# Performance work log

Measured on AMD Instinct MI355X. Metric: run time of the kernel, lower is better.

The kernel has to match this reference:

```python
import jax, jax.numpy as jnp
from jax import lax
import numpy as np

NUM_HEADS = 8
EPS = 1e-5


def _ln_c(x, g, b):
    # channel-first layernorm: x (B,C,S), normalize over C
    m = jnp.mean(x, axis=1, keepdims=True)
    v = jnp.var(x, axis=1, keepdims=True)
    return (x - m) / jnp.sqrt(v + EPS) * g[None, :, None] + b[None, :, None]


def _ln(x, g, b):
    m = jnp.mean(x, axis=-1, keepdims=True)
    v = jnp.var(x, axis=-1, keepdims=True)
    return (x - m) / jnp.sqrt(v + EPS) * g + b


def _sepconv(x, dw_w, dw_b, bn_s, bn_b, pw_w, pw_b, stride, pad):
    # depthwise conv -> eval BatchNorm (affine) -> ReLU -> pointwise conv
    C = x.shape[1]
    y = lax.conv_general_dilated(x, dw_w[:, None, :], (stride,), [(pad, pad)],
                                 dimension_numbers=('NCH', 'OIH', 'NCH'),
                                 feature_group_count=C)
    y = y + dw_b[None, :, None]
    y = jax.nn.relu(y * bn_s[None, :, None] + bn_b[None, :, None])
    return jnp.einsum('oc,bcs->bos', pw_w, y) + pw_b[None, :, None]


def setup_inputs() -> dict:
    T, B, C, S, K, F = 2, 8, 256, 1024, 5, 1024
    keys = iter(jax.random.split(jax.random.key(0), 64))
    def rn(*shape):
        return jax.random.normal(next(keys), shape, jnp.float32)
    def w(*shape):
        return rn(*shape) * 0.05
    ones = lambda *s: jnp.ones(s, jnp.float32)
    zeros = lambda *s: jnp.zeros(s, jnp.float32)
    return {
        'inp': rn(T, B, C, S), 'cls': rn(B, C),
        'ln1_g': ones(T, C), 'ln1_b': zeros(T, C),
        'q_dw_w': w(T, C, K), 'q_dw_b': w(T, C), 'q_bn_s': ones(T, C), 'q_bn_b': zeros(T, C),
        'q_pw_w': w(T, C, C), 'q_pw_b': w(T, C),
        'kv_dw_w': w(T, C, K), 'kv_dw_b': w(T, C), 'kv_bn_s': ones(T, C), 'kv_bn_b': zeros(T, C),
        'kv_pw_w': w(T, 2 * C, C), 'kv_pw_b': w(T, 2 * C),
        'wq_cls': w(C, C), 'bq_cls': w(C),
        'ln1c_g': ones(C), 'ln1c_b': zeros(C),
        'wout': w(C, C), 'bout': w(C),
        'ff1_dw_w': w(T, C, K), 'ff1_dw_b': w(T, C), 'ff1_bn_s': ones(T, C), 'ff1_bn_b': zeros(T, C),
        'ff1_pw_w': w(T, F, C), 'ff1_pw_b': w(T, F),
        'ff2_dw_w': w(T, F, K), 'ff2_dw_b': w(T, F), 'ff2_bn_s': ones(T, F), 'ff2_bn_b': zeros(T, F),
        'ff2_pw_w': w(T, C, F), 'ff2_pw_b': w(T, C),
        'ln2_g': ones(T, C), 'ln2_b': zeros(T, C),
        'ln2c_g': ones(C), 'ln2c_b': zeros(C),
        'wff1': w(F, C), 'bff1': w(F), 'wff2': w(C, F), 'bff2': w(C),
    }


def reference(inp, cls, ln1_g, ln1_b, q_dw_w, q_dw_b, q_bn_s, q_bn_b, q_pw_w, q_pw_b,
              kv_dw_w, kv_dw_b, kv_bn_s, kv_bn_b, kv_pw_w, kv_pw_b, wq_cls, bq_cls,
              ln1c_g, ln1c_b, wout, bout, ff1_dw_w, ff1_dw_b, ff1_bn_s, ff1_bn_b,
              ff1_pw_w, ff1_pw_b, ff2_dw_w, ff2_dw_b, ff2_bn_s, ff2_bn_b, ff2_pw_w,
              ff2_pw_b, ln2_g, ln2_b, ln2c_g, ln2c_b, wff1, bff1, wff2, bff2):
    T, B, C, S = inp.shape
    H = NUM_HEADS
    hd = C // H
    pad_q = q_dw_w.shape[-1] // 2
    pad_f = ff1_dw_w.shape[-1] // 2

    def qkv_tf(x, g, b, qdw, qdb, qbs, qbb, qpw, qpb, kdw, kdb, kbs, kbb, kpw, kpb):
        xn = _ln_c(x, g, b)
        q = _sepconv(xn, qdw, qdb, qbs, qbb, qpw, qpb, 1, pad_q)
        kv = _sepconv(xn, kdw, kdb, kbs, kbb, kpw, kpb, 2, pad_q)
        k, v = jnp.split(kv, 2, axis=1)
        return xn, q, k, v

    xn, q, k, v = jax.vmap(qkv_tf)(inp, ln1_g, ln1_b, q_dw_w, q_dw_b, q_bn_s, q_bn_b,
                                   q_pw_w, q_pw_b, kv_dw_w, kv_dw_b, kv_bn_s, kv_bn_b,
                                   kv_pw_w, kv_pw_b)

    cls_norm = _ln(cls, ln1c_g, ln1c_b)
    q_cls = (cls_norm @ wq_cls.T + bq_cls)[:, :, None]  # (B,C,1)

    def cat_tf(a):  # (T,B,C,L) -> (B,C,T*L), timeframe order preserved
        return jnp.transpose(a, (1, 2, 0, 3)).reshape(B, C, -1)

    query = jnp.concatenate([cat_tf(q), q_cls], axis=2)  # (B,C,Lq)
    qh = query.reshape(B, H, hd, -1)
    kh = cat_tf(k).reshape(B, H, hd, -1)
    vh = cat_tf(v).reshape(B, H, hd, -1)

    logits = jnp.einsum('bhdq,bhdk->bhqk', qh, kh) / float(np.sqrt(hd))
    attn = jax.nn.softmax(logits, axis=-1)
    av = jnp.einsum('bhqk,bhdk->bhqd', attn, vh)         # (B,H,Lq,hd)
    av = jnp.transpose(av, (0, 2, 1, 3)).reshape(B, -1, C)  # (B,Lq,C)
    attn_out = jnp.transpose(av @ wout.T + bout, (0, 2, 1))  # (B,C,Lq)
    attn_tf = jnp.transpose(attn_out[:, :, :-1].reshape(B, C, T, S), (2, 0, 1, 3))
    attn_cls = attn_out[:, :, -1]

    def ffn_tf(xn_i, a_i, g2, b2, d1w, d1b, s1, bb1, p1w, p1b, d2w, d2b, s2, bb2, p2w, p2b):
        x = xn_i + a_i
        h = _sepconv(_ln_c(x, g2, b2), d1w, d1b, s1, bb1, p1w, p1b, 1, pad_f)
        h = jax.nn.relu(h)
        h = _sepconv(h, d2w, d2b, s2, bb2, p2w, p2b, 1, pad_f)
        return x + h

    y = jax.vmap(ffn_tf)(xn, attn_tf, ln2_g, ln2_b, ff1_dw_w, ff1_dw_b, ff1_bn_s,
                         ff1_bn_b, ff1_pw_w, ff1_pw_b, ff2_dw_w, ff2_dw_b, ff2_bn_s,
                         ff2_bn_b, ff2_pw_w, ff2_pw_b)

    xc = cls_norm + attn_cls
    hc = jax.nn.relu(_ln(xc, ln2c_g, ln2c_b) @ wff1.T + bff1) @ wff2.T + bff2
    y_cls = xc + hc
    return (y, y_cls)
```

## Files before the change

### kernel.cpp

```cpp
#include <hip/hip_runtime.h>
#include <hip/hip_bf16.h>

typedef __hip_bfloat16 bf16;
using short8 = __attribute__((ext_vector_type(8))) short;
using float4v = __attribute__((ext_vector_type(4))) float;

__device__ __forceinline__ float b2f(bf16 x) { return __bfloat162float(x); }
__device__ __forceinline__ bf16 f2b(float x) { return __float2bfloat16(x); }
__device__ __forceinline__ short f2bs(float v) {
  bf16 x = f2b(v);
  return *reinterpret_cast<short*>(&x);
}

__device__ int g_dt;
__device__ bf16 g_R1[16777216];
__device__ bf16 g_R2[4194304];
__device__ float g_m1[16384], g_r1[16384];
__device__ float g_m2[16384], g_r2[16384];
__device__ float g_clsnorm[2048], g_qcls[2048], g_attncls[2048];
__device__ float g_xc[2048], g_xcn[2048], g_hcls[8192];

#define KT_OFF 4194304L

__device__ __forceinline__ float LD(const void* p, size_t i, int dt) {
  return dt ? b2f(((const bf16*)p)[i]) : ((const float*)p)[i];
}
__device__ __forceinline__ void ST(void* p, size_t i, int dt, float v) {
  if (dt) ((bf16*)p)[i] = f2b(v);
  else ((float*)p)[i] = v;
}

__global__ void sniff_kernel(const unsigned int* w) {
  g_dt = (w[0] == 0x3F803F80u) ? 1 : 0;
}

template <int MODE>
__global__ __launch_bounds__(256) void ln_stats_kernel(const void* xext) {
  const int C = 256, S = 1024;
  int dt = g_dt;
  int z = blockIdx.z;
  int si = threadIdx.x & 63;
  int s = blockIdx.x * 64 + si;
  int cg = threadIdx.x >> 6;
  size_t base = (size_t)z * C * S;
  float sum = 0.f, sq = 0.f;
  for (int i = 0; i < 64; ++i) {
    int c = cg * 64 + i;
    float v = (MODE == 0) ? LD(xext, base + (size_t)c * S + s, dt)
                          : b2f(g_R2[base + (size_t)c * S + s]);
    sum += v; sq += v * v;
  }
  __shared__ float sS[4][64], sQ[4][64];
  sS[cg][si] = sum;
  sQ[cg][si] = sq;
  __syncthreads();
  if (cg == 0) {
    float tot = sS[0][si] + sS[1][si] + sS[2][si] + sS[3][si];
    float tq = sQ[0][si] + sQ[1][si] + sQ[2][si] + sQ[3][si];
    float m = tot / (float)C;
    float var = tq / (float)C - m * m;
    int sg = blockIdx.x * 64 + si;
    if (MODE == 0) {
      g_m1[(size_t)z * S + sg] = m;
      g_r1[(size_t)z * S + sg] = rsqrtf(var + 1e-5f);
    } else {
      g_m2[(size_t)z * S + sg] = m;
      g_r2[(size_t)z * S + sg] = rsqrtf(var + 1e-5f);
    }
  }
}

template <int ACT, bool RESID, int STRIDE, bool HASLN, int WHICHLN,
          bool SRCEXT, bool DSTEXT, int OUTMODE>
__global__ __launch_bounds__(256) void mfma_gemm_dw_kernel(
    const void* __restrict__ W, long wOff, long wStrideT,
    const void* __restrict__ srcExt, int srcSel, long srcOff,
    const void* __restrict__ dww, const void* __restrict__ dwb,
    const void* __restrict__ bns, const void* __restrict__ bnb, long pOff,
    long pStrideT,
    const void* __restrict__ bias, long bOff, long bStrideT,
    void* __restrict__ dstExt, int dstSel, long dstOff,
    long resOff,
    int O, int Cin, int N, int Sin, int B,
    const void* __restrict__ lnG, const void* __restrict__ lnB, long lnOff,
    int lnStride, int zOff) {
  constexpr int SRCW = STRIDE * 128 + 4;
  int dt = g_dt;
  int z = blockIdx.z;
  int t = z / B;
  long wB = wOff + (size_t)t * wStrideT;
  long bB = bOff + (size_t)t * bStrideT;
  long pB = pOff + (size_t)t * pStrideT;
  const bf16* srcI = nullptr;
  size_t srcBase = (size_t)z * Cin * Sin;
  if (!SRCEXT) srcI = (srcSel == 1 ? g_R1 : g_R2) + srcOff + srcBase;
  int o0 = blockIdx.y * 128;
  int n0 = blockIdx.x * 128;
  int tid = threadIdx.x;
  int lane = tid & 63, w = tid >> 6;
  int wr = (w & 1) * 64, wc = (w >> 1) * 64;
  int m = lane & 15, quad = lane >> 4;

  __shared__ alignas(16) bf16 sW[128][40];
  __shared__ alignas(16) bf16 sXb[128][40];
  __shared__ bf16 sSrc[32][SRCW];
  __shared__ float sDW[32][8];

  float4v acc[4][4];
#pragma unroll
  for (int a = 0; a < 4; ++a)
#pragma unroll
    for (int c = 0; c < 4; ++c) acc[a][c] = {0.f, 0.f, 0.f, 0.f};

  for (int k0 = 0; k0 < Cin; k0 += 32) {
    if (dt == 0) {
      const float* Wf = (const float*)W;
#pragma unroll
      for (int l = 0; l < 4; ++l) {
        int i = l * 256 + tid;
        int oo = i >> 3, kk = (i & 7) * 4;
        const float4 f =
            *(const float4*)&Wf[wB + (size_t)(o0 + oo) * Cin + k0 + kk];
        sW[oo][kk + 0] = f2b(f.x);
        sW[oo][kk + 1] = f2b(f.y);
        sW[oo][kk + 2] = f2b(f.z);
        sW[oo][kk + 3] = f2b(f.w);
      }
    } else {
      const bf16* Wb = (const bf16*)W;
#pragma unroll
      for (int l = 0; l < 2; ++l) {
        int i = l * 256 + tid;
        int oo = i >> 2, kk = (i & 3) * 8;
        *(short8*)&sW[oo][kk] =
            *(const short8*)&Wb[wB + (size_t)(o0 + oo) * Cin + k0 + kk];
      }
    }
    {
      int rr = tid >> 3, f = tid & 7;
      if (rr < 32) {
        int c = k0 + rr;
        float v;
        if (f < 5) v = LD(dww, pB * 5 + c * 5 + f, dt);
        else if (f == 5) v = LD(dwb, pB + c, dt);
        else if (f == 6) v = LD(bns, pB + c, dt);
        else v = LD(bnb, pB + c, dt);
        sDW[rr][f] = v;
      }
    }
    for (int i = tid; i < 32 * SRCW; i += 256) {
      int row = i / SRCW, col = i - row * SRCW;
      int s = n0 * STRIDE - 2 + col;
      float v = 0.f;
      if (s >= 0 && s < Sin) {
        if (SRCEXT) v = LD(srcExt, srcBase + (size_t)(k0 + row) * Sin + s, dt);
        else v = b2f(srcI[(size_t)(k0 + row) * Sin + s]);
        if (HASLN) {
          const float* M = WHICHLN ? g_m2 : g_m1;
          const float* Rr = WHICHLN ? g_r2 : g_r1;
          size_t si = (size_t)(z + zOff) * Sin + s;
          float gg = LD(lnG, lnOff + t * lnStride + k0 + row, dt);
          float bbv = LD(lnB, lnOff + t * lnStride + k0 + row, dt);
          v = (v - M[si]) * Rr[si] * gg + bbv;
        }
      }
      sSrc[row][col] = f2b(v);
    }
    __syncthreads();
#pragma unroll
    for (int l = 0; l < 16; ++l) {
      int i = l * 256 + tid;
      int kk = i >> 7, nn = i & 127;
      float a = sDW[kk][5];
#pragma unroll
      for (int j = 0; j < 5; ++j)
        a += sDW[kk][j] * b2f(sSrc[kk][nn * STRIDE + j]);
      sXb[nn][kk] = f2b(fmaxf(a * sDW[kk][6] + sDW[kk][7], 0.f));
    }
    __syncthreads();
    short8 af[4], fb[4];
#pragma unroll
    for (int a = 0; a < 4; ++a)
      af[a] = *(const short8*)&sW[wr + a * 16 + m][quad * 8];
#pragma unroll
    for (int c = 0; c < 4; ++c)
      fb[c] = *(const short8*)&sXb[wc + c * 16 + m][quad * 8];
#pragma unroll
    for (int a = 0; a < 4; ++a)
#pragma unroll
      for (int c = 0; c < 4; ++c)
        acc[a][c] = __builtin_amdgcn_mfma_f32_16x16x32_bf16(af[a], fb[c],
                                                            acc[a][c], 0, 0, 0);
    __syncthreads();
  }

  const bf16* resp = RESID ? (g_R2 + resOff + (size_t)z * O * N) : nullptr;
  bf16* dstI = nullptr;
  if (!DSTEXT) dstI = (dstSel == 1 ? g_R1 : g_R2) + dstOff;
#pragma unroll
  for (int a = 0; a < 4; ++a) {
    float bv[4];
#pragma unroll
    for (int r = 0; r < 4; ++r)
      bv[r] = LD(bias, bB + o0 + wr + a * 16 + quad * 4 + r, dt);
#pragma unroll
    for (int c = 0; c < 4; ++c) {
      int n = n0 + wc + c * 16 + m;
#pragma unroll
      for (int r = 0; r < 4; ++r) {
        int o = o0 + wr + a * 16 + quad * 4 + r;
        float v = acc[a][c][r] + bv[r];
        if (ACT == 1) v = fmaxf(v, 0.f);
        if (OUTMODE == 1) {
          g_R1[((size_t)z * N + n) * 256 + o] =
              f2b(v * 0.17677669529663687f);
        } else if (OUTMODE == 2) {
          if (o < 256)
            g_R1[KT_OFF + ((size_t)z * N + n) * 256 + o] = f2b(v);
          else
            dstI[(size_t)z * O * N + (size_t)o * N + n] = f2b(v);
        } else {
          if (RESID) v += b2f(resp[(size_t)o * N + n]);
          size_t oidx = (size_t)z * O * N + (size_t)o * N + n;
          if (DSTEXT) ST(dstExt, dstOff + oidx, dt, v);
          else dstI[oidx] = f2b(v);
        }
      }
    }
  }
}

__global__ __launch_bounds__(256) void mfma_wout_kernel(
    const void* __restrict__ W, const bf16* __restrict__ avT,
    const void* __restrict__ bias) {
  const int Cin = 256;
  int dt = g_dt;
  int z = blockIdx.z;
  int o0 = blockIdx.y * 128;
  int n0 = blockIdx.x * 128;
  int tid = threadIdx.x;
  int lane = tid & 63, w = tid >> 6;
  int wr = (w & 1) * 64, wc = (w >> 1) * 64;
  int m = lane & 15, quad = lane >> 4;

  __shared__ alignas(16) bf16 sW[128][40];
  __shared__ alignas(16) bf16 sXb[128][40];

  float4v acc[4][4];
#pragma unroll
  for (int a = 0; a < 4; ++a)
#pragma unroll
    for (int c = 0; c < 4; ++c) acc[a][c] = {0.f, 0.f, 0.f, 0.f};

  for (int k0 = 0; k0 < Cin; k0 += 32) {
    if (dt == 0) {
      const float* Wf = (const float*)W;
#pragma unroll
      for (int l = 0; l < 4; ++l) {
        int i = l * 256 + tid;
        int oo = i >> 3, kk = (i & 7) * 4;
        const float4 f = *(const float4*)&Wf[(size_t)(o0 + oo) * Cin + k0 + kk];
        sW[oo][kk + 0] = f2b(f.x);
        sW[oo][kk + 1] = f2b(f.y);
        sW[oo][kk + 2] = f2b(f.z);
        sW[oo][kk + 3] = f2b(f.w);
      }
    } else {
      const bf16* Wb = (const bf16*)W;
#pragma unroll
      for (int l = 0; l < 2; ++l) {
        int i = l * 256 + tid;
        int oo = i >> 2, kk = (i & 3) * 8;
        *(short8*)&sW[oo][kk] =
            *(const short8*)&Wb[(size_t)(o0 + oo) * Cin + k0 + kk];
      }
    }
#pragma unroll
    for (int l = 0; l < 2; ++l) {
      int i = l * 256 + tid;
      int nn = i >> 2, part = i & 3;
      int n = n0 + nn;
      short8 vv = (short8)0;
      if (n < 2049)
        vv = *(const short8*)&avT[((size_t)z * 2049 + n) * 256 + k0 + part * 8];
      *(short8*)&sXb[nn][part * 8] = vv;
    }
    __syncthreads();
    short8 af[4], fb[4];
#pragma unroll
    for (int a = 0; a < 4; ++a)
      af[a] = *(const short8*)&sW[wr + a * 16 + m][quad * 8];
#pragma unroll
    for (int c = 0; c < 4; ++c)
      fb[c] = *(const short8*)&sXb[wc + c * 16 + m][quad * 8];
#pragma unroll
    for (int a = 0; a < 4; ++a)
#pragma unroll
      for (int c = 0; c < 4; ++c)
        acc[a][c] = __builtin_amdgcn_mfma_f32_16x16x32_bf16(af[a], fb[c],
                                                            acc[a][c], 0, 0, 0);
    __syncthreads();
  }

#pragma unroll
  for (int a = 0; a < 4; ++a) {
    float bv[4];
#pragma unroll
    for (int r = 0; r < 4; ++r)
      bv[r] = LD(bias, o0 + wr + a * 16 + quad * 4 + r, dt);
#pragma unroll
    for (int c = 0; c < 4; ++c) {
      int n = n0 + wc + c * 16 + m;
#pragma unroll
      for (int r = 0; r < 4; ++r) {
        int o = o0 + wr + a * 16 + quad * 4 + r;
        float v = acc[a][c][r] + bv[r];
        if (n < 2048) g_R1[((size_t)z * 256 + o) * 2048 + n] = f2b(v);
        else if (n == 2048) g_attncls[z * 256 + o] = v;
      }
    }
  }
}

__global__ __launch_bounds__(256) void flash_mfma_kernel(bf16* __restrict__ avT,
                                                         int B) {
  const int b = blockIdx.z, h = blockIdx.y;
  const int n0 = blockIdx.x * 64;
  const int tid = threadIdx.x;
  const int lane = tid & 63, w = tid >> 6;
  const int m = lane & 15, quad = lane >> 4;

  __shared__ alignas(16) bf16 sP[4][16][72];

  const bf16* QT = g_R1;
  const bf16* KT = g_R1 + KT_OFF;

  short8 aq = (short8)0;
  {
    int qglob = n0 + w * 16 + m;
    if (qglob < 2048) {
      int t = qglob >> 10, s = qglob & 1023;
      aq = *(const short8*)&QT[((size_t)((t * 8 + b) * 1024 + s)) * 256 +
                               h * 32 + quad * 8];
    } else if (qglob == 2048) {
      short8 u;
#pragma unroll
      for (int j = 0; j < 8; ++j)
        u[j] = f2bs(g_qcls[b * 256 + h * 32 + quad * 8 + j] *
                    0.17677669529663687f);
      aq = u;
    }
  }

  float4v accO[2];
  accO[0] = {0.f, 0.f, 0.f, 0.f};
  accO[1] = {0.f, 0.f, 0.f, 0.f};
  float lsum[4] = {0.f, 0.f, 0.f, 0.f};
  float mrow[4] = {-1e30f, -1e30f, -1e30f, -1e30f};

  for (int kt = 0; kt < 16; ++kt) {
    int t = kt >> 3;
    int s0 = (kt * 64) & 511;
    size_t kbase = (size_t)(t * 8 + b) * 512 * 256;
    short8 fbk[4];
#pragma unroll
    for (int c = 0; c < 4; ++c)
      fbk[c] = *(const short8*)&KT[kbase + (size_t)(s0 + c * 16 + m) * 256 +
                                   h * 32 + quad * 8];
    float4v sacc[4];
#pragma unroll
    for (int c = 0; c < 4; ++c) {
      sacc[c] = {0.f, 0.f, 0.f, 0.f};
      sacc[c] =
          __builtin_amdgcn_mfma_f32_16x16x32_bf16(aq, fbk[c], sacc[c], 0, 0, 0);
    }
    float alpha[4];
#pragma unroll
    for (int r = 0; r < 4; ++r) {
      float v = fmaxf(fmaxf(sacc[0][r], sacc[1][r]),
                      fmaxf(sacc[2][r], sacc[3][r]));
#pragma unroll
      for (int off = 1; off < 16; off <<= 1) v = fmaxf(v, __shfl_xor(v, off));
      float mn = fmaxf(mrow[r], v);
      alpha[r] = __expf(mrow[r] - mn);
      mrow[r] = mn;
      lsum[r] *= alpha[r];
    }
#pragma unroll
    for (int d2 = 0; d2 < 2; ++d2)
#pragma unroll
      for (int r = 0; r < 4; ++r) accO[d2][r] *= alpha[r];
    float rsum[4] = {0.f, 0.f, 0.f, 0.f};
#pragma unroll
    for (int c = 0; c < 4; ++c)
#pragma unroll
      for (int r = 0; r < 4; ++r) {
        float p = __expf(sacc[c][r] - mrow[r]);
        sacc[c][r] = p;
        rsum[r] += p;
      }
#pragma unroll
    for (int r = 0; r < 4; ++r) {
      float v = rsum[r];
#pragma unroll
      for (int off = 1; off < 16; off <<= 1) v += __shfl_xor(v, off);
      lsum[r] += v;
    }
#pragma unroll
    for (int c = 0; c < 4; ++c)
#pragma unroll
      for (int r = 0; r < 4; ++r)
        sP[w][quad * 4 + r][c * 16 + m] = f2b(sacc[c][r]);
    __syncthreads();
    short8 afp0 = *(const short8*)&sP[w][m][quad * 8];
    short8 afp1 = *(const short8*)&sP[w][m][32 + quad * 8];
#pragma unroll
    for (int d2 = 0; d2 < 2; ++d2) {
      size_t vrow =
          ((size_t)(t * 8 + b) * 512 + 256 + h * 32 + d2 * 16 + m) * 512;
      short8 fv0 = *(const short8*)&g_R2[vrow + s0 + quad * 8];
      short8 fv1 = *(const short8*)&g_R2[vrow + s0 + 32 + quad * 8];
      accO[d2] =
          __builtin_amdgcn_mfma_f32_16x16x32_bf16(afp0, fv0, accO[d2], 0, 0, 0);
      accO[d2] =
          __builtin_amdgcn_mfma_f32_16x16x32_bf16(afp1, fv1, accO[d2], 0, 0, 0);
    }
    __syncthreads();
  }

#pragma unroll
  for (int r = 0; r < 4; ++r) {
    int n = n0 + w * 16 + quad * 4 + r;
    if (n < 2049) {
      float inv = 1.f / lsum[r];
#pragma unroll
      for (int d2 = 0; d2 < 2; ++d2)
        avT[((size_t)b * 2049 + n) * 256 + h * 32 + d2 * 16 + m] =
            f2b(accO[d2][r] * inv);
    }
  }
}

__global__ __launch_bounds__(256) void build_x_kernel(
    const void* __restrict__ inp, const void* __restrict__ g1,
    const void* __restrict__ b1) {
  int dt = g_dt;
  size_t idx = (size_t)blockIdx.x * 256 + threadIdx.x;
  int s = idx & 1023;
  int c = (int)(idx >> 10) & 255;
  int z = (int)(idx >> 18);
  int t = z >> 3, b = z & 7;
  size_t si = (size_t)z * 1024 + s;
  float v = (LD(inp, idx, dt) - g_m1[si]) * g_r1[si] *
                LD(g1, t * 256 + c, dt) +
            LD(b1, t * 256 + c, dt);
  v += b2f(g_R1[((size_t)(b * 256 + c)) * 2048 + t * 1024 + s]);
  g_R2[idx] = f2b(v);
}

template <int MODE>
__global__ __launch_bounds__(256) void row_ln_kernel(
    const void* __restrict__ xin, const void* __restrict__ g,
    const void* __restrict__ bb) {
  int dt = g_dt;
  int r = blockIdx.x, c = threadIdx.x;
  float v = (MODE == 0) ? LD(xin, r * 256 + c, dt) : g_xc[r * 256 + c];
  __shared__ float sA[256], sB[256];
  sA[c] = v;
  sB[c] = v * v;
  __syncthreads();
  for (int off = 128; off > 0; off >>= 1) {
    if (c < off) { sA[c] += sA[c + off]; sB[c] += sB[c + off]; }
    __syncthreads();
  }
  float m = sA[0] / 256.f;
  float var = sB[0] / 256.f - m * m;
  float rs = rsqrtf(var + 1e-5f);
  float o = (v - m) * rs * LD(g, c, dt) + LD(bb, c, dt);
  if (MODE == 0) g_clsnorm[r * 256 + c] = o;
  else g_xcn[r * 256 + c] = o;
}

template <int STAGE>
__global__ __launch_bounds__(256) void cls_mm_kernel(
    const void* __restrict__ W, const void* __restrict__ bias,
    void* __restrict__ out, long outOff, int Cin, int O) {
  int dt = g_dt;
  int b = blockIdx.y;
  int o = blockIdx.x * 256 + threadIdx.x;
  __shared__ float sx[1024];
  const float* xin = (STAGE == 0) ? g_clsnorm : (STAGE == 1 ? g_xcn : g_hcls);
  for (int c = threadIdx.x; c < Cin; c += 256) sx[c] = xin[b * Cin + c];
  __syncthreads();
  float acc = LD(bias, o, dt);
  for (int c = 0; c < Cin; ++c) acc += LD(W, (size_t)o * Cin + c, dt) * sx[c];
  if (STAGE == 0) g_qcls[b * O + o] = acc;
  else if (STAGE == 1) g_hcls[b * O + o] = fmaxf(acc, 0.f);
  else ST(out, outOff + b * O + o, dt, acc + g_xc[b * O + o]);
}

__global__ void xc_kernel() {
  int b = blockIdx.x, c = threadIdx.x;
  g_xc[b * 256 + c] = g_clsnorm[b * 256 + c] + g_attncls[b * 256 + c];
}

extern "C" void kernel_launch(void* const* d_in, const int* in_sizes, int n_in,
                              void* d_out, int out_size, void* d_ws,
                              size_t ws_size, hipStream_t stream) {
  constexpr int T = 2, B = 8, C = 256, S = 1024, F = 1024;
  constexpr size_t N_TBCS = (size_t)T * B * C * S;

  const void* in_inp = d_in[0];
  const void* in_cls = d_in[1];
  const void* ln1_g = d_in[2];
  const void* ln1_b = d_in[3];
  const void* q_dw_w = d_in[4];
  const void* q_dw_b = d_in[5];
  const void* q_bn_s = d_in[6];
  const void* q_bn_b = d_in[7];
  const void* q_pw_w = d_in[8];
  const void* q_pw_b = d_in[9];
  const void* kv_dw_w = d_in[10];
  const void* kv_dw_b = d_in[11];
  const void* kv_bn_s = d_in[12];
  const void* kv_bn_b = d_in[13];
  const void* kv_pw_w = d_in[14];
  const void* kv_pw_b = d_in[15];
  const void* wq_cls = d_in[16];
  const void* bq_cls = d_in[17];
  const void* ln1c_g = d_in[18];
  const void* ln1c_b = d_in[19];
  const void* wout = d_in[20];
  const void* bout = d_in[21];
  const void* ff1_dw_w = d_in[22];
  const void* ff1_dw_b = d_in[23];
  const void* ff1_bn_s = d_in[24];
  const void* ff1_bn_b = d_in[25];
  const void* ff1_pw_w = d_in[26];
  const void* ff1_pw_b = d_in[27];
  const void* ff2_dw_w = d_in[28];
  const void* ff2_dw_b = d_in[29];
  const void* ff2_bn_s = d_in[30];
  const void* ff2_bn_b = d_in[31];
  const void* ff2_pw_w = d_in[32];
  const void* ff2_pw_b = d_in[33];
  const void* ln2_g = d_in[34];
  const void* ln2_b = d_in[35];
  const void* ln2c_g = d_in[36];
  const void* ln2c_b = d_in[37];
  const void* wff1 = d_in[38];
  const void* bff1 = d_in[39];
  const void* wff2 = d_in[40];
  const void* bff2 = d_in[41];

  bf16* avT = (bf16*)d_out;

  dim3 blk256(256);

  sniff_kernel<<<1, 1, 0, stream>>>((const unsigned int*)ln1_g);

  ln_stats_kernel<0><<<dim3(16, 1, 16), blk256, 0, stream>>>(in_inp);

  mfma_gemm_dw_kernel<0, false, 1, true, 0, true, false, 1>
      <<<dim3(8, 2, 16), blk256, 0, stream>>>(
          q_pw_w, 0L, (long)C * C, in_inp, 0, 0L, q_dw_w, q_dw_b, q_bn_s,
          q_bn_b, 0L, C, q_pw_b, 0L, C, nullptr, 1, 0L, 0L, C, C, S, S, B,
          ln1_g, ln1_b, 0L, C, 0);

  mfma_gemm_dw_kernel<0, false, 2, true, 0, true, false, 2>
      <<<dim3(4, 4, 16), blk256, 0, stream>>>(
          kv_pw_w, 0L, (long)2 * C * C, in_inp, 0, 0L, kv_dw_w, kv_dw_b,
          kv_bn_s, kv_bn_b, 0L, C, kv_pw_b, 0L, 2 * C, nullptr, 2, 0L, 0L,
          2 * C, C, S / 2, S, B, ln1_g, ln1_b, 0L, C, 0);

  row_ln_kernel<0><<<dim3(B), blk256, 0, stream>>>(in_cls, ln1c_g, ln1c_b);
  cls_mm_kernel<0><<<dim3(1, B), blk256, 0, stream>>>(wq_cls, bq_cls, nullptr,
                                                      0L, C, C);

  flash_mfma_kernel<<<dim3(33, 8, B), blk256, 0, stream>>>(avT, B);

  mfma_wout_kernel<<<dim3(17, 2, B), blk256, 0, stream>>>(wout, avT, bout);

  xc_kernel<<<dim3(B), blk256, 0, stream>>>();
  row_ln_kernel<1><<<dim3(B), blk256, 0, stream>>>(nullptr, ln2c_g, ln2c_b);
  cls_mm_kernel<1><<<dim3(F / 256, B), blk256, 0, stream>>>(wff1, bff1,
                                                            nullptr, 0L, C, F);
  cls_mm_kernel<2><<<dim3(1, B), blk256, 0, stream>>>(
      wff2, bff2, d_out, (long)N_TBCS, F, C);

  build_x_kernel<<<dim3(N_TBCS / 256), blk256, 0, stream>>>(in_inp, ln1_g,
                                                            ln1_b);

  ln_stats_kernel<1><<<dim3(16, 1, 16), blk256, 0, stream>>>(nullptr);

  mfma_gemm_dw_kernel<1, false, 1, true, 1, false, false, 0>
      <<<dim3(8, 8, 16), blk256, 0, stream>>>(
          ff1_pw_w, 0L, (long)F * C, nullptr, 2, 0L, ff1_dw_w, ff1_dw_b,
          ff1_bn_s, ff1_bn_b, 0L, C, ff1_pw_b, 0L, F, nullptr, 1, 0L, 0L, F,
          C, S, S, B, ln2_g, ln2_b, 0L, C, 0);
  mfma_gemm_dw_kernel<0, true, 1, false, 0, false, true, 0>
      <<<dim3(8, 2, 16), blk256, 0, stream>>>(
          ff2_pw_w, 0L, (long)C * F, nullptr, 1, 0L, ff2_dw_w, ff2_dw_b,
          ff2_bn_s, ff2_bn_b, 0L, F, ff2_pw_b, 0L, C, d_out, 0, 0L, 0L, C, F,
          S, S, B, nullptr, nullptr, 0L, 0, 0);
}
```

Baseline: 1.240 ms.

## Halve GEMM output tile to 64 rows, cache LN stats, vectorize depthwise stores

The fused depthwise+pointwise GEMM kernels and the wout GEMM now use 64-row output tiles instead of 128, doubling grid size in the output dimension to raise occupancy and block count. Per-column LayerNorm mean/rstd and per-channel gamma/beta are staged into shared memory instead of being reloaded per element. The depthwise conv stage now computes 8 channels per thread and writes them as one vector store into the shared B tile. The trade-off is that the depthwise conv and source loading are recomputed twice as often across the extra output-row blocks.

```diff
diff --git a/kernel.cpp b/kernel.cpp
--- a/kernel.cpp
+++ b/kernel.cpp
@@ -94,21 +94,40 @@
   const bf16* srcI = nullptr;
   size_t srcBase = (size_t)z * Cin * Sin;
   if (!SRCEXT) srcI = (srcSel == 1 ? g_R1 : g_R2) + srcOff + srcBase;
-  int o0 = blockIdx.y * 128;
+  int o0 = blockIdx.y * 64;
   int n0 = blockIdx.x * 128;
   int tid = threadIdx.x;
   int lane = tid & 63, w = tid >> 6;
-  int wr = (w & 1) * 64, wc = (w >> 1) * 64;
+  int wr = (w & 1) * 32, wc = (w >> 1) * 64;
   int m = lane & 15, quad = lane >> 4;
 
-  __shared__ alignas(16) bf16 sW[128][40];
+  __shared__ alignas(16) bf16 sW[64][40];
   __shared__ alignas(16) bf16 sXb[128][40];
   __shared__ bf16 sSrc[32][SRCW];
   __shared__ float sDW[32][8];
-
-  float4v acc[4][4];
-#pragma unroll
-  for (int a = 0; a < 4; ++a)
+  __shared__ float sLNg[32], sLNb[32];
+  __shared__ float sMs[SRCW], sRs[SRCW];
+
+  if (HASLN) {
+    const float* M = WHICHLN ? g_m2 : g_m1;
+    const float* Rr = WHICHLN ? g_r2 : g_r1;
+    for (int i = tid; i < SRCW; i += 256) {
+      int s = n0 * STRIDE - 2 + i;
+      float mv = 0.f, rv = 0.f;
+      if (s >= 0 && s < Sin) {
+        size_t si = (size_t)(z + zOff) * Sin + s;
+        mv = M[si];
+        rv = Rr[si];
+      }
+      sMs[i] = mv;
+      sRs[i] = rv;
+    }
+    __syncthreads();
+  }
+
+  float4v acc[2][4];
+#pragma unroll
+  for (int a = 0; a < 2; ++a)
 #pragma unroll
     for (int c = 0; c < 4; ++c) acc[a][c] = {0.f, 0.f, 0.f, 0.f};
 
@@ -116,7 +135,7 @@
     if (dt == 0) {
       const float* Wf = (const float*)W;
 #pragma unroll
-      for (int l = 0; l < 4; ++l) {
+      for (int l = 0; l < 2; ++l) {
         int i = l * 256 + tid;
         int oo = i >> 3, kk = (i & 7) * 4;
         const float4 f =
@@ -128,13 +147,9 @@
       }
     } else {
       const bf16* Wb = (const bf16*)W;
-#pragma unroll
-      for (int l = 0; l < 2; ++l) {
-        int i = l * 256 + tid;
-        int oo = i >> 2, kk = (i & 3) * 8;
-        *(short8*)&sW[oo][kk] =
-            *(const short8*)&Wb[wB + (size_t)(o0 + oo) * Cin + k0 + kk];
-      }
+      int oo = tid >> 2, kk = (tid & 3) * 8;
+      *(short8*)&sW[oo][kk] =
+          *(const short8*)&Wb[wB + (size_t)(o0 + oo) * Cin + k0 + kk];
     }
     {
       int rr = tid >> 3, f = tid & 7;
@@ -148,6 +163,10 @@
         sDW[rr][f] = v;
       }
     }
+    if (HASLN && tid < 32) {
+      sLNg[tid] = LD(lnG, lnOff + t * lnStride + k0 + tid, dt);
+      sLNb[tid] = LD(lnB, lnOff + t * lnStride + k0 + tid, dt);
+    }
     for (int i = tid; i < 32 * SRCW; i += 256) {
       int row = i / SRCW, col = i - row * SRCW;
       int s = n0 * STRIDE - 2 + col;
@@ -155,38 +174,37 @@
       if (s >= 0 && s < Sin) {
         if (SRCEXT) v = LD(srcExt, srcBase + (size_t)(k0 + row) * Sin + s, dt);
         else v = b2f(srcI[(size_t)(k0 + row) * Sin + s]);
-        if (HASLN) {
-          const float* M = WHICHLN ? g_m2 : g_m1;
-          const float* Rr = WHICHLN ? g_r2 : g_r1;
-          size_t si = (size_t)(z + zOff) * Sin + s;
-          float gg = LD(lnG, lnOff + t * lnStride + k0 + row, dt);
-          float bbv = LD(lnB, lnOff + t * lnStride + k0 + row, dt);
-          v = (v - M[si]) * Rr[si] * gg + bbv;
-        }
+        if (HASLN) v = (v - sMs[col]) * sRs[col] * sLNg[row] + sLNb[row];
       }
       sSrc[row][col] = f2b(v);
     }
     __syncthreads();
 #pragma unroll
-    for (int l = 0; l < 16; ++l) {
-      int i = l * 256 + tid;
-      int kk = i >> 7, nn = i & 127;
-      float a = sDW[kk][5];
-#pragma unroll
-      for (int j = 0; j < 5; ++j)
-        a += sDW[kk][j] * b2f(sSrc[kk][nn * STRIDE + j]);
-      sXb[nn][kk] = f2b(fmaxf(a * sDW[kk][6] + sDW[kk][7], 0.f));
-    }
-    __syncthreads();
-    short8 af[4], fb[4];
-#pragma unroll
-    for (int a = 0; a < 4; ++a)
+    for (int l = 0; l < 2; ++l) {
+      int j = l * 256 + tid;
+      int nn = j & 127, ch = j >> 7;
+      short8 outv;
+#pragma unroll
+      for (int jj = 0; jj < 8; ++jj) {
+        int kk = ch * 8 + jj;
+        float a = sDW[kk][5];
+#pragma unroll
+        for (int tap = 0; tap < 5; ++tap)
+          a += sDW[kk][tap] * b2f(sSrc[kk][nn * STRIDE + tap]);
+        outv[jj] = f2bs(fmaxf(a * sDW[kk][6] + sDW[kk][7], 0.f));
+      }
+      *(short8*)&sXb[nn][ch * 8] = outv;
+    }
+    __syncthreads();
+    short8 af[2], fb[4];
+#pragma unroll
+    for (int a = 0; a < 2; ++a)
       af[a] = *(const short8*)&sW[wr + a * 16 + m][quad * 8];
 #pragma unroll
     for (int c = 0; c < 4; ++c)
       fb[c] = *(const short8*)&sXb[wc + c * 16 + m][quad * 8];
 #pragma unroll
-    for (int a = 0; a < 4; ++a)
+    for (int a = 0; a < 2; ++a)
 #pragma unroll
       for (int c = 0; c < 4; ++c)
         acc[a][c] = __builtin_amdgcn_mfma_f32_16x16x32_bf16(af[a], fb[c],
@@ -198,7 +216,7 @@
   bf16* dstI = nullptr;
   if (!DSTEXT) dstI = (dstSel == 1 ? g_R1 : g_R2) + dstOff;
 #pragma unroll
-  for (int a = 0; a < 4; ++a) {
+  for (int a = 0; a < 2; ++a) {
     float bv[4];
 #pragma unroll
     for (int r = 0; r < 4; ++r)
@@ -236,19 +254,19 @@
   const int Cin = 256;
   int dt = g_dt;
   int z = blockIdx.z;
-  int o0 = blockIdx.y * 128;
+  int o0 = blockIdx.y * 64;
   int n0 = blockIdx.x * 128;
   int tid = threadIdx.x;
   int lane = tid & 63, w = tid >> 6;
-  int wr = (w & 1) * 64, wc = (w >> 1) * 64;
+  int wr = (w & 1) * 32, wc = (w >> 1) * 64;
   int m = lane & 15, quad = lane >> 4;
 
-  __shared__ alignas(16) bf16 sW[128][40];
+  __shared__ alignas(16) bf16 sW[64][40];
   __shared__ alignas(16) bf16 sXb[128][40];
 
-  float4v acc[4][4];
-#pragma unroll
-  for (int a = 0; a < 4; ++a)
+  float4v acc[2][4];
+#pragma unroll
+  for (int a = 0; a < 2; ++a)
 #pragma unroll
     for (int c = 0; c < 4; ++c) acc[a][c] = {0.f, 0.f, 0.f, 0.f};
 
@@ -256,7 +274,7 @@
     if (dt == 0) {
       const float* Wf = (const float*)W;
 #pragma unroll
-      for (int l = 0; l < 4; ++l) {
+      for (int l = 0; l < 2; ++l) {
         int i = l * 256 + tid;
         int oo = i >> 3, kk = (i & 7) * 4;
         const float4 f = *(const float4*)&Wf[(size_t)(o0 + oo) * Cin + k0 + kk];
@@ -267,34 +285,30 @@
       }
     } else {
       const bf16* Wb = (const bf16*)W;
-#pragma unroll
-      for (int l = 0; l < 2; ++l) {
-        int i = l * 256 + tid;
-        int oo = i >> 2, kk = (i & 3) * 8;
-        *(short8*)&sW[oo][kk] =
-            *(const short8*)&Wb[(size_t)(o0 + oo) * Cin + k0 + kk];
-      }
+      int oo = tid >> 2, kk = (tid & 3) * 8;
+      *(short8*)&sW[oo][kk] =
+          *(const short8*)&Wb[(size_t)(o0 + oo) * Cin + k0 + kk];
     }
 #pragma unroll
     for (int l = 0; l < 2; ++l) {
       int i = l * 256 + tid;
-      int nn = i >> 2, part = i & 3;
+      int nn = i >> 2, ch = i & 3;
       int n = n0 + nn;
       short8 vv = (short8)0;
       if (n < 2049)
-        vv = *(const short8*)&avT[((size_t)z * 2049 + n) * 256 + k0 + part * 8];
-      *(short8*)&sXb[nn][part * 8] = vv;
-    }
-    __syncthreads();
-    short8 af[4], fb[4];
-#pragma unroll
-    for (int a = 0; a < 4; ++a)
+        vv = *(const short8*)&avT[((size_t)z * 2049 + n) * 256 + k0 + ch * 8];
+      *(short8*)&sXb[nn][ch * 8] = vv;
+    }
+    __syncthreads();
+    short8 af[2], fb[4];
+#pragma unroll
+    for (int a = 0; a < 2; ++a)
       af[a] = *(const short8*)&sW[wr + a * 16 + m][quad * 8];
 #pragma unroll
     for (int c = 0; c < 4; ++c)
       fb[c] = *(const short8*)&sXb[wc + c * 16 + m][quad * 8];
 #pragma unroll
-    for (int a = 0; a < 4; ++a)
+    for (int a = 0; a < 2; ++a)
 #pragma unroll
       for (int c = 0; c < 4; ++c)
         acc[a][c] = __builtin_amdgcn_mfma_f32_16x16x32_bf16(af[a], fb[c],
@@ -303,7 +317,7 @@
   }
 
 #pragma unroll
-  for (int a = 0; a < 4; ++a) {
+  for (int a = 0; a < 2; ++a) {
     float bv[4];
 #pragma unroll
     for (int r = 0; r < 4; ++r)
@@ -562,13 +576,13 @@
   ln_stats_kernel<0><<<dim3(16, 1, 16), blk256, 0, stream>>>(in_inp);
 
   mfma_gemm_dw_kernel<0, false, 1, true, 0, true, false, 1>
-      <<<dim3(8, 2, 16), blk256, 0, stream>>>(
+      <<<dim3(8, 4, 16), blk256, 0, stream>>>(
           q_pw_w, 0L, (long)C * C, in_inp, 0, 0L, q_dw_w, q_dw_b, q_bn_s,
           q_bn_b, 0L, C, q_pw_b, 0L, C, nullptr, 1, 0L, 0L, C, C, S, S, B,
           ln1_g, ln1_b, 0L, C, 0);
 
   mfma_gemm_dw_kernel<0, false, 2, true, 0, true, false, 2>
-      <<<dim3(4, 4, 16), blk256, 0, stream>>>(
+      <<<dim3(4, 8, 16), blk256, 0, stream>>>(
           kv_pw_w, 0L, (long)2 * C * C, in_inp, 0, 0L, kv_dw_w, kv_dw_b,
           kv_bn_s, kv_bn_b, 0L, C, kv_pw_b, 0L, 2 * C, nullptr, 2, 0L, 0L,
           2 * C, C, S / 2, S, B, ln1_g, ln1_b, 0L, C, 0);
@@ -579,7 +593,7 @@
 
   flash_mfma_kernel<<<dim3(33, 8, B), blk256, 0, stream>>>(avT, B);
 
-  mfma_wout_kernel<<<dim3(17, 2, B), blk256, 0, stream>>>(wout, avT, bout);
+  mfma_wout_kernel<<<dim3(17, 4, B), blk256, 0, stream>>>(wout, avT, bout);
 
   xc_kernel<<<dim3(B), blk256, 0, stream>>>();
   row_ln_kernel<1><<<dim3(B), blk256, 0, stream>>>(nullptr, ln2c_g, ln2c_b);
@@ -594,12 +608,12 @@
   ln_stats_kernel<1><<<dim3(16, 1, 16), blk256, 0, stream>>>(nullptr);
 
   mfma_gemm_dw_kernel<1, false, 1, true, 1, false, false, 0>
-      <<<dim3(8, 8, 16), blk256, 0, stream>>>(
+      <<<dim3(8, 16, 16), blk256, 0, stream>>>(
           ff1_pw_w, 0L, (long)F * C, nullptr, 2, 0L, ff1_dw_w, ff1_dw_b,
           ff1_bn_s, ff1_bn_b, 0L, C, ff1_pw_b, 0L, F, nullptr, 1, 0L, 0L, F,
           C, S, S, B, ln2_g, ln2_b, 0L, C, 0);
   mfma_gemm_dw_kernel<0, true, 1, false, 0, false, true, 0>
-      <<<dim3(8, 2, 16), blk256, 0, stream>>>(
+      <<<dim3(8, 4, 16), blk256, 0, stream>>>(
           ff2_pw_w, 0L, (long)C * F, nullptr, 1, 0L, ff2_dw_w, ff2_dw_b,
           ff2_bn_s, ff2_bn_b, 0L, F, ff2_pw_b, 0L, C, d_out, 0, 0L, 0L, C, F,
           S, S, B, nullptr, nullptr, 0L, 0, 0);
```

New measurement: 1.261 ms. Within noise of the previous version (+1.8%).
